# Kernel tuning notes

Hardware: AMD Instinct MI355X
Metric: run time of the kernel (lower is better)

The kernel has to match this reference:

```python
import jax, jax.numpy as jnp
import numpy as np

B, T, C, H = 4, 2048, 768, 12
HD = C // H  # 64
EPS = 1e-5


def layer_norm(x, g, b):
    mu = jnp.mean(x, axis=-1, keepdims=True)
    var = jnp.var(x, axis=-1, keepdims=True)
    return (x - mu) * jax.lax.rsqrt(var + EPS) * g + b


def setup_inputs() -> dict:
    key = jax.random.key(0)
    ks = jax.random.split(key, 14)
    s_c = 1.0 / np.sqrt(C)
    s_4c = 1.0 / np.sqrt(4 * C)
    return {
        "x": jax.random.normal(ks[0], (B, T, C), jnp.float32),
        # per-head Q/K/V projections stacked over heads [H, C, HD]
        "wq": jax.random.uniform(ks[1], (H, C, HD), jnp.float32, -s_c, s_c),
        "bq": jnp.zeros((H, HD), jnp.float32),
        "wk": jax.random.uniform(ks[2], (H, C, HD), jnp.float32, -s_c, s_c),
        "bk": jnp.zeros((H, HD), jnp.float32),
        "wv": jax.random.uniform(ks[3], (H, C, HD), jnp.float32, -s_c, s_c),
        "bv": jnp.zeros((H, HD), jnp.float32),
        "w_proj": jax.random.uniform(ks[4], (C, C), jnp.float32, -s_c, s_c),
        "b_proj": jnp.zeros((C,), jnp.float32),
        "w1": jax.random.uniform(ks[5], (C, 4 * C), jnp.float32, -s_c, s_c),
        "b1": jnp.zeros((4 * C,), jnp.float32),
        "w2": jax.random.uniform(ks[6], (4 * C, C), jnp.float32, -s_4c, s_4c),
        "b2": jnp.zeros((C,), jnp.float32),
        "g1": jnp.ones((C,), jnp.float32),
        "beta1": jnp.zeros((C,), jnp.float32),
        "g2": jnp.ones((C,), jnp.float32),
        "beta2": jnp.zeros((C,), jnp.float32),
    }


def reference(x, wq, bq, wk, bk, wv, bv, w_proj, b_proj, w1, b1, w2, b2, g1, beta1, g2, beta2):
    # --- attention sublayer ---
    h = layer_norm(x, g1, beta1)
    q = jnp.einsum('btc,hcd->bhtd', h, wq) + bq[None, :, None, :]
    k = jnp.einsum('btc,hcd->bhtd', h, wk) + bk[None, :, None, :]
    v = jnp.einsum('btc,hcd->bhtd', h, wv) + bv[None, :, None, :]
    # NOTE: source applies NO 1/sqrt(head_size) scaling
    scores = jnp.einsum('bhtd,bhsd->bhts', q, k)  # [B,H,T,T]
    causal = jnp.tril(jnp.ones((T, T), bool))
    scores = jnp.where(causal, scores, -jnp.inf)
    wei = jax.nn.softmax(scores, axis=-1)
    attn = jnp.einsum('bhts,bhsd->bhtd', wei, v)  # [B,H,T,HD]
    attn = attn.transpose(0, 2, 1, 3).reshape(B, T, C)  # concat heads
    x = x + attn @ w_proj + b_proj
    # --- MLP sublayer ---
    h2 = layer_norm(x, g2, beta2)
    x = x + jax.nn.relu(h2 @ w1 + b1) @ w2 + b2
    return x
```

## Files before the change

kernel.cpp:

```cpp
#include <hip/hip_runtime.h>
#include <hip/hip_bf16.h>
#include <math.h>

#define BB 4
#define TT 2048
#define CC 768
#define HH 12
#define HDIM 64
#define C4 3072
#define MM (BB*TT)
#define EPSL 1e-5f

typedef __bf16 bf16x8 __attribute__((ext_vector_type(8)));
typedef __bf16 bf16x4 __attribute__((ext_vector_type(4)));
typedef float f32x4 __attribute__((ext_vector_type(4)));

__device__ __forceinline__ ushort f2bf(float f) {
    union { float f; unsigned u; } v; v.f = f;
    unsigned r = v.u + 0x7fffu + ((v.u >> 16) & 1u);
    return (ushort)(r >> 16);
}

__device__ __forceinline__ void glds16(const void* g, void* l) {
    __builtin_amdgcn_global_load_lds(
        (const __attribute__((address_space(1))) void*)g,
        (__attribute__((address_space(3))) void*)l, 16, 0, 0);
}

#define WVM(N) asm volatile("s_waitcnt vmcnt(" #N ")" ::: "memory")
#define WLG0   asm volatile("s_waitcnt lgkmcnt(0)" ::: "memory")

__device__ __forceinline__ void pbar() {
    __builtin_amdgcn_sched_barrier(0);
    __builtin_amdgcn_s_barrier();
    __builtin_amdgcn_sched_barrier(0);
}

__global__ __launch_bounds__(256) void ln_k(const float* __restrict__ X,
                                            const float* __restrict__ G,
                                            const float* __restrict__ Be,
                                            ushort* __restrict__ O)
{
    int row = blockIdx.x;
    const float* xr = X + (size_t)row * CC;
    int t = threadIdx.x;
    float v0 = xr[t], v1 = xr[t + 256], v2 = xr[t + 512];
    float s  = v0 + v1 + v2;
    float sq = v0*v0 + v1*v1 + v2*v2;
    #pragma unroll
    for (int off = 32; off; off >>= 1) {
        s  += __shfl_xor(s,  off);
        sq += __shfl_xor(sq, off);
    }
    __shared__ float red[8];
    int wv = t >> 6, ln = t & 63;
    if (ln == 0) { red[wv] = s; red[4 + wv] = sq; }
    __syncthreads();
    s  = red[0] + red[1] + red[2] + red[3];
    sq = red[4] + red[5] + red[6] + red[7];
    float mu  = s * (1.0f / CC);
    float var = sq * (1.0f / CC) - mu * mu;
    float rs  = rsqrtf(var + EPSL);
    ushort* orow = O + (size_t)row * CC;
    orow[t]       = f2bf((v0 - mu) * rs * G[t]       + Be[t]);
    orow[t + 256] = f2bf((v1 - mu) * rs * G[t + 256] + Be[t + 256]);
    orow[t + 512] = f2bf((v2 - mu) * rs * G[t + 512] + Be[t + 512]);
}

__global__ __launch_bounds__(256) void ln_add_k(float* __restrict__ X,
                                                const float* __restrict__ P,
                                                const float* __restrict__ G,
                                                const float* __restrict__ Be,
                                                ushort* __restrict__ O)
{
    int row = blockIdx.x;
    float* xr = X + (size_t)row * CC;
    const float* pr = P + (size_t)row * CC;
    int t = threadIdx.x;
    float v0 = xr[t]       + pr[t];
    float v1 = xr[t + 256] + pr[t + 256];
    float v2 = xr[t + 512] + pr[t + 512];
    xr[t] = v0; xr[t + 256] = v1; xr[t + 512] = v2;
    float s  = v0 + v1 + v2;
    float sq = v0*v0 + v1*v1 + v2*v2;
    #pragma unroll
    for (int off = 32; off; off >>= 1) {
        s  += __shfl_xor(s,  off);
        sq += __shfl_xor(sq, off);
    }
    __shared__ float red[8];
    int wv = t >> 6, ln = t & 63;
    if (ln == 0) { red[wv] = s; red[4 + wv] = sq; }
    __syncthreads();
    s  = red[0] + red[1] + red[2] + red[3];
    sq = red[4] + red[5] + red[6] + red[7];
    float mu  = s * (1.0f / CC);
    float var = sq * (1.0f / CC) - mu * mu;
    float rs  = rsqrtf(var + EPSL);
    ushort* orow = O + (size_t)row * CC;
    orow[t]       = f2bf((v0 - mu) * rs * G[t]       + Be[t]);
    orow[t + 256] = f2bf((v1 - mu) * rs * G[t + 256] + Be[t + 256]);
    orow[t + 512] = f2bf((v2 - mu) * rs * G[t + 512] + Be[t + 512]);
}

__global__ __launch_bounds__(256) void addto_k(float* __restrict__ o,
                                               const float* __restrict__ p,
                                               int n4)
{
    int i = blockIdx.x * 256 + threadIdx.x;
    int stride = gridDim.x * 256;
    for (; i < n4; i += stride) {
        float4 a = ((const float4*)o)[i];
        float4 b = ((const float4*)p)[i];
        a.x += b.x; a.y += b.y; a.z += b.z; a.w += b.w;
        ((float4*)o)[i] = a;
    }
}

template<int MODE>
__global__ __launch_bounds__(256) void repack_k(const float* __restrict__ W,
                                                ushort* __restrict__ WT,
                                                int K, int N, int outStride)
{
    __shared__ float tl[64][65];
    int n0 = blockIdx.x * 64, k0 = blockIdx.y * 64;
    int c = threadIdx.x & 63, rr = threadIdx.x >> 6;
    #pragma unroll
    for (int i = 0; i < 16; ++i) {
        int r = i * 4 + rr;
        float v;
        if (MODE == 0) v = W[(size_t)(k0 + r) * N + n0 + c];
        else           v = W[((size_t)(n0 >> 6) * CC + k0 + r) * 64 + c];
        tl[r][c] = v;
    }
    __syncthreads();
    #pragma unroll
    for (int i = 0; i < 16; ++i) {
        int r = i * 4 + rr;
        WT[(size_t)(n0 + r) * outStride + k0 + c] = f2bf(tl[c][r]);
    }
}

template<int EPI>
__global__ __launch_bounds__(512, 2) void gemm8p(
    const ushort* __restrict__ A, const ushort* __restrict__ BT,
    int M, int N, int K,
    void* __restrict__ ov0, void* __restrict__ ov1, void* __restrict__ ov2,
    const float* __restrict__ bias0, const float* __restrict__ bias1,
    const float* __restrict__ bias2,
    const float* __restrict__ resid, ushort* __restrict__ obf,
    float* __restrict__ part)
{
    __shared__ ushort lds[2][2][256 * 64];

    int nbx = gridDim.x;
    int nwg = nbx * gridDim.y * gridDim.z;
    int orig = (blockIdx.z * gridDim.y + blockIdx.y) * nbx + blockIdx.x;
    int cpx = nwg >> 3;
    int swz = (orig & 7) * cpx + (orig >> 3);
    int zi = swz / (nbx * gridDim.y);
    int rem = swz - zi * nbx * gridDim.y;
    int bn = rem % nbx, bm = rem / nbx;

    int tid = threadIdx.x;
    int lane = tid & 63;
    int w = tid >> 6;
    int wrow = (w >> 2) * 128, wcol = (w & 3) * 64;
    int fr = lane & 15, kh = lane >> 4;
    int rxor = (fr & 7) * 8;

    const size_t aR0 = (size_t)bm * 256;
    const size_t bR0 = (size_t)bn * 256;
    const int Ksl = K / (int)gridDim.z;
    const int koff = zi * Ksl;
    const int nt = Ksl >> 6;

    int srow = tid >> 3;
    int scol = (tid & 7) * 8;
    int gcol = koff + (scol ^ ((srow & 7) * 8));

    f32x4 acc[8][4] = {};

    {
        glds16(BT + (bR0 +   0 + srow) * K + gcol, &lds[0][1][(  0 + srow) * 64 + scol]);
        glds16(BT + (bR0 +  64 + srow) * K + gcol, &lds[0][1][( 64 + srow) * 64 + scol]);
        glds16(BT + (bR0 + 128 + srow) * K + gcol, &lds[0][1][(128 + srow) * 64 + scol]);
        glds16(BT + (bR0 + 192 + srow) * K + gcol, &lds[0][1][(192 + srow) * 64 + scol]);
        glds16(A  + (aR0 +   0 + srow) * K + gcol, &lds[0][0][(  0 + srow) * 64 + scol]);
        glds16(A  + (aR0 + 128 + srow) * K + gcol, &lds[0][0][(128 + srow) * 64 + scol]);
        glds16(A  + (aR0 +  64 + srow) * K + gcol, &lds[0][0][( 64 + srow) * 64 + scol]);
        glds16(A  + (aR0 + 192 + srow) * K + gcol, &lds[0][0][(192 + srow) * 64 + scol]);
    }
    WVM(2);
    pbar();

    for (int t = 0; t < nt; ++t) {
        int slot = t & 1, nslot = slot ^ 1;
        int kst = gcol + ((t + 1) << 6);
        bool st = (t + 1) < nt;
        const ushort* Asl = &lds[slot][0][0];
        const ushort* Bsl = &lds[slot][1][0];
        bf16x8 aF[4][2];
        #pragma unroll
        for (int p = 0; p < 4; ++p) {
            const int rh = p >> 1, ch = p & 1;
            if (ch == 0) {
                #pragma unroll
                for (int i = 0; i < 4; ++i)
                    #pragma unroll
                    for (int k2 = 0; k2 < 2; ++k2) {
                        int R = wrow + rh * 64 + i * 16 + fr;
                        aF[i][k2] = *(const bf16x8*)&Asl[R * 64 + ((k2 * 32 + kh * 8) ^ rxor)];
                    }
            }
            bf16x8 bF[2][2];
            #pragma unroll
            for (int j2 = 0; j2 < 2; ++j2)
                #pragma unroll
                for (int k2 = 0; k2 < 2; ++k2) {
                    int Rb = wcol + ch * 32 + j2 * 16 + fr;
                    bF[j2][k2] = *(const bf16x8*)&Bsl[Rb * 64 + ((k2 * 32 + kh * 8) ^ rxor)];
                }
            if (st) {
                if (p == 0) {
                    glds16(BT + (bR0 +   0 + srow) * K + kst, &lds[nslot][1][(  0 + srow) * 64 + scol]);
                    glds16(BT + (bR0 +  64 + srow) * K + kst, &lds[nslot][1][( 64 + srow) * 64 + scol]);
                    glds16(BT + (bR0 + 128 + srow) * K + kst, &lds[nslot][1][(128 + srow) * 64 + scol]);
                    glds16(BT + (bR0 + 192 + srow) * K + kst, &lds[nslot][1][(192 + srow) * 64 + scol]);
                } else if (p == 1) {
                    glds16(A  + (aR0 +   0 + srow) * K + kst, &lds[nslot][0][(  0 + srow) * 64 + scol]);
                    glds16(A  + (aR0 + 128 + srow) * K + kst, &lds[nslot][0][(128 + srow) * 64 + scol]);
                    glds16(A  + (aR0 +  64 + srow) * K + kst, &lds[nslot][0][( 64 + srow) * 64 + scol]);
                    glds16(A  + (aR0 + 192 + srow) * K + kst, &lds[nslot][0][(192 + srow) * 64 + scol]);
                }
            }
            __builtin_amdgcn_s_setprio(1);
            #pragma unroll
            for (int i = 0; i < 4; ++i)
                #pragma unroll
                for (int j2 = 0; j2 < 2; ++j2)
                    #pragma unroll
                    for (int k2 = 0; k2 < 2; ++k2)
                        acc[rh * 4 + i][ch * 2 + j2] = __builtin_amdgcn_mfma_f32_16x16x32_bf16(
                            aF[i][k2], bF[j2][k2], acc[rh * 4 + i][ch * 2 + j2], 0, 0, 0);
            __builtin_amdgcn_s_setprio(0);
            if (p == 1) { if (st) { WVM(8); } else { WVM(0); } }
            else if (p == 3) { if (st) { WVM(2); } }
            WLG0;
            pbar();
        }
    }

    if (gridDim.z > 1 && zi > 0) {
        #pragma unroll
        for (int ri = 0; ri < 8; ++ri) {
            int row0 = bm * 256 + wrow + ri * 16 + kh * 4;
            #pragma unroll
            for (int cj = 0; cj < 4; ++cj) {
                int col = bn * 256 + wcol + cj * 16 + fr;
                #pragma unroll
                for (int r = 0; r < 4; ++r)
                    part[(size_t)(row0 + r) * N + col] = acc[ri][cj][r];
            }
        }
    } else if (EPI == 1) {
        int seg = bn / 3;
        ushort* op = (ushort*)(seg == 0 ? ov0 : (seg == 1 ? ov1 : ov2));
        const float* bsp = seg == 0 ? bias0 : (seg == 1 ? bias1 : bias2);
        int cb = (bn - seg * 3) * 256 + wcol;
        int h = cb >> 6;
        #pragma unroll
        for (int ri = 0; ri < 8; ++ri) {
            int row0 = bm * 256 + wrow + ri * 16 + kh * 4;
            int b = row0 >> 11;
            int t0 = row0 & (TT - 1);
            #pragma unroll
            for (int cj = 0; cj < 4; ++cj) {
                int d = cj * 16 + fr;
                float bsv = bsp[h * 64 + d];
                #pragma unroll
                for (int r = 0; r < 4; ++r)
                    op[((size_t)(b * HH + h) * TT + t0 + r) * 64 + d] =
                        f2bf(acc[ri][cj][r] + bsv);
            }
        }
    } else if (EPI == 2) {
        float* o0 = (float*)ov0;
        #pragma unroll
        for (int ri = 0; ri < 8; ++ri) {
            int row0 = bm * 256 + wrow + ri * 16 + kh * 4;
            #pragma unroll
            for (int cj = 0; cj < 4; ++cj) {
                int col = bn * 256 + wcol + cj * 16 + fr;
                float bsv = bias0[col];
                #pragma unroll
                for (int r = 0; r < 4; ++r) {
                    size_t idx = (size_t)(row0 + r) * N + col;
                    o0[idx] = acc[ri][cj][r] + bsv + resid[idx];
                }
            }
        }
    } else {
        #pragma unroll
        for (int ri = 0; ri < 8; ++ri) {
            int row0 = bm * 256 + wrow + ri * 16 + kh * 4;
            #pragma unroll
            for (int cj = 0; cj < 4; ++cj) {
                int col = bn * 256 + wcol + cj * 16 + fr;
                float bsv = bias0[col];
                #pragma unroll
                for (int r = 0; r < 4; ++r) {
                    float v = fmaxf(acc[ri][cj][r] + bsv, 0.f);
                    obf[(size_t)(row0 + r) * N + col] = f2bf(v);
                }
            }
        }
    }
}

__global__ __launch_bounds__(256) void vtrans_k(const ushort* __restrict__ V,
                                                ushort* __restrict__ Vt)
{
    __shared__ ushort tl[64][72];
    int blk = blockIdx.x;
    int tt = blk & 31, bh = blk >> 5;
    size_t base = (size_t)bh * TT * 64;
    int t0 = tt * 64;
    int e = threadIdx.x;
    int rr = e >> 3, cc8 = (e & 7) * 8;
    #pragma unroll
    for (int p = 0; p < 2; ++p) {
        int t = p * 32 + rr;
        *(uint4*)&tl[t][cc8] = *(const uint4*)&V[base + (size_t)(t0 + t) * 64 + cc8];
    }
    __syncthreads();
    #pragma unroll
    for (int p = 0; p < 2; ++p) {
        int d = p * 32 + rr;
        ushort tmp[8];
        #pragma unroll
        for (int i = 0; i < 8; ++i) tmp[i] = tl[cc8 + i][d];
        *(uint4*)&Vt[base + (size_t)d * TT + t0 + cc8] = *(uint4*)tmp;
    }
}

__global__ __launch_bounds__(256) void attn_k(const ushort* __restrict__ Q,
                                              const ushort* __restrict__ Kb,
                                              const ushort* __restrict__ Vt,
                                              ushort* __restrict__ Ob)
{
    __shared__ ushort Kl[64][72];
    __shared__ ushort Vl[64][72];
    __shared__ ushort Pl[4][16][68];

    int orig = blockIdx.x;
    int swz = (orig & 7) * 192 + (orig >> 3);
    int qt = 31 - (swz & 31);
    int bh = swz >> 5;
    int b = bh / HH, h = bh - b * HH;
    int q0 = qt * 64;
    int tid = threadIdx.x, lane = tid & 63, w = tid >> 6;
    int c = lane & 15, g = lane >> 4;
    size_t base = (size_t)bh * TT * 64;
    int srow = tid >> 3, scol = (tid & 7) * 8;
    const float LOG2E = 1.44269504088896340736f;

    bf16x8 aq[2];
    #pragma unroll
    for (int kc = 0; kc < 2; ++kc) {
        bf16x8 raw = *(const bf16x8*)&Q[base + (size_t)(q0 + w * 16 + c) * 64 + kc * 32 + g * 8];
        #pragma unroll
        for (int e = 0; e < 8; ++e)
            raw[e] = (__bf16)((float)raw[e] * LOG2E);
        aq[kc] = raw;
    }

    f32x4 oa[4] = {};
    float mrun[4] = {-INFINITY, -INFINITY, -INFINITY, -INFINITY};
    float lrun[4] = {0.f, 0.f, 0.f, 0.f};

    for (int kv0 = 0; kv0 <= q0; kv0 += 64) {
        __syncthreads();
        #pragma unroll
        for (int p = 0; p < 2; ++p) {
            int r = p * 32 + srow;
            *(uint4*)&Kl[r][scol] = *(const uint4*)&Kb[base + (size_t)(kv0 + r) * 64 + scol];
            *(uint4*)&Vl[r][scol] = *(const uint4*)&Vt[base + (size_t)r * TT + kv0 + scol];
        }
        __syncthreads();

        f32x4 sa[4] = {};
        #pragma unroll
        for (int kc = 0; kc < 2; ++kc)
            #pragma unroll
            for (int j = 0; j < 4; ++j) {
                bf16x8 kf = *(const bf16x8*)&Kl[j * 16 + c][kc * 32 + g * 8];
                sa[j] = __builtin_amdgcn_mfma_f32_16x16x32_bf16(aq[kc], kf, sa[j], 0, 0, 0);
            }

        if (kv0 == q0) {
            #pragma unroll
            for (int j = 0; j < 4; ++j)
                #pragma unroll
                for (int r = 0; r < 4; ++r)
                    if (j * 16 + c > w * 16 + g * 4 + r) sa[j][r] = -1e30f;
        }

        float vlmax = sa[0][0];
        #pragma unroll
        for (int j = 0; j < 4; ++j)
            #pragma unroll
            for (int r = 0; r < 4; ++r) vlmax = fmaxf(vlmax, sa[j][r]);
        float mmin = fminf(fminf(mrun[0], mrun[1]), fminf(mrun[2], mrun[3]));
        if (!__all(vlmax <= mmin + 11.5f)) {
            #pragma unroll
            for (int r = 0; r < 4; ++r) {
                float m0 = fmaxf(fmaxf(sa[0][r], sa[1][r]), fmaxf(sa[2][r], sa[3][r]));
                #pragma unroll
                for (int off = 8; off; off >>= 1) m0 = fmaxf(m0, __shfl_xor(m0, off));
                float mnew = fmaxf(mrun[r], m0);
                float sc = __builtin_amdgcn_exp2f(mrun[r] - mnew);
                lrun[r] *= sc;
                #pragma unroll
                for (int j = 0; j < 4; ++j) oa[j][r] *= sc;
                mrun[r] = mnew;
            }
        }
        #pragma unroll
        for (int r = 0; r < 4; ++r) {
            float ps = 0.f;
            #pragma unroll
            for (int j = 0; j < 4; ++j) {
                float p = __builtin_amdgcn_exp2f(sa[j][r] - mrun[r]);
                sa[j][r] = p;
                ps += p;
            }
            lrun[r] += ps;
        }

        #pragma unroll
        for (int r = 0; r < 4; ++r)
            #pragma unroll
            for (int j = 0; j < 4; ++j)
                Pl[w][g * 4 + r][j * 16 + c] = (ushort)__builtin_bit_cast(unsigned short, (__bf16)sa[j][r]);

        bf16x8 pf[2];
        #pragma unroll
        for (int kc = 0; kc < 2; ++kc) {
            bf16x4 lo = *(const bf16x4*)&Pl[w][c][kc * 32 + g * 8];
            bf16x4 hi = *(const bf16x4*)&Pl[w][c][kc * 32 + g * 8 + 4];
            pf[kc] = __builtin_shufflevector(lo, hi, 0, 1, 2, 3, 4, 5, 6, 7);
        }

        #pragma unroll
        for (int kc = 0; kc < 2; ++kc)
            #pragma unroll
            for (int j = 0; j < 4; ++j) {
                bf16x8 vf = *(const bf16x8*)&Vl[j * 16 + c][kc * 32 + g * 8];
                oa[j] = __builtin_amdgcn_mfma_f32_16x16x32_bf16(pf[kc], vf, oa[j], 0, 0, 0);
            }
    }

    float inv[4];
    #pragma unroll
    for (int r = 0; r < 4; ++r) {
        float l = lrun[r];
        #pragma unroll
        for (int off = 8; off; off >>= 1) l += __shfl_xor(l, off);
        inv[r] = 1.0f / l;
    }
    size_t orow = (size_t)b * TT + q0 + w * 16;
    #pragma unroll
    for (int j = 0; j < 4; ++j)
        #pragma unroll
        for (int r = 0; r < 4; ++r) {
            float v = oa[j][r] * inv[r];
            Ob[(orow + g * 4 + r) * CC + h * 64 + j * 16 + c] = f2bf(v);
        }
}

extern "C" void kernel_launch(void* const* d_in, const int* in_sizes, int n_in,
                              void* d_out, int out_size, void* d_ws, size_t ws_size,
                              hipStream_t stream)
{
    const float* x   = (const float*)d_in[0];
    const float* wq  = (const float*)d_in[1];
    const float* bq  = (const float*)d_in[2];
    const float* wk  = (const float*)d_in[3];
    const float* bk  = (const float*)d_in[4];
    const float* wvw = (const float*)d_in[5];
    const float* bv  = (const float*)d_in[6];
    const float* wp  = (const float*)d_in[7];
    const float* bp  = (const float*)d_in[8];
    const float* w1  = (const float*)d_in[9];
    const float* b1  = (const float*)d_in[10];
    const float* w2  = (const float*)d_in[11];
    const float* b2  = (const float*)d_in[12];
    const float* g1  = (const float*)d_in[13];
    const float* be1 = (const float*)d_in[14];
    const float* g2  = (const float*)d_in[15];
    const float* be2 = (const float*)d_in[16];

    float* out = (float*)d_out;
    const size_t S = (size_t)MM * CC;

    ushort* wsu   = (ushort*)d_ws;
    ushort* WTqkv = wsu;
    ushort* WTp   = WTqkv + (size_t)2304 * 768;
    ushort* WT1   = WTp   + (size_t)768 * 768;
    ushort* WT2   = WT1   + (size_t)3072 * 768;
    ushort* hbf   = WT2   + (size_t)768 * 3072;
    ushort* attnb = hbf   + S;
    ushort* qb    = attnb + S;
    ushort* kb    = qb + S;
    ushort* vb    = kb + S;
    ushort* vtb   = vb + S;
    ushort* midb  = qb;
    float*  part_proj = (float*)qb;
    float*  part_w2   = (float*)hbf;

    dim3 rg(12, 12);
    repack_k<1><<<rg, 256, 0, stream>>>(wq,  WTqkv,                      768, 768, 768);
    repack_k<1><<<rg, 256, 0, stream>>>(wk,  WTqkv + (size_t)768*768,    768, 768, 768);
    repack_k<1><<<rg, 256, 0, stream>>>(wvw, WTqkv + (size_t)2*768*768,  768, 768, 768);
    repack_k<0><<<rg, 256, 0, stream>>>(wp,  WTp, 768, 768, 768);
    repack_k<0><<<dim3(48, 12), 256, 0, stream>>>(w1, WT1, 768, 3072, 768);
    repack_k<0><<<dim3(12, 48), 256, 0, stream>>>(w2, WT2, 3072, 768, 3072);

    ln_k<<<MM, 256, 0, stream>>>(x, g1, be1, hbf);
    gemm8p<1><<<dim3(9, 32, 1), 512, 0, stream>>>(hbf, WTqkv, MM, 2304, CC,
        qb, kb, vb, bq, bk, bv, nullptr, nullptr, nullptr);
    vtrans_k<<<48 * 32, 256, 0, stream>>>(vb, vtb);
    attn_k<<<48 * 32, 256, 0, stream>>>(qb, kb, vtb, attnb);
    gemm8p<2><<<dim3(3, 32, 2), 512, 0, stream>>>(attnb, WTp, MM, CC, CC,
        out, nullptr, nullptr, bp, nullptr, nullptr, x, nullptr, part_proj);

    ln_add_k<<<MM, 256, 0, stream>>>(out, part_proj, g2, be2, hbf);
    gemm8p<3><<<dim3(12, 32, 1), 512, 0, stream>>>(hbf, WT1, MM, C4, CC,
        nullptr, nullptr, nullptr, b1, nullptr, nullptr, nullptr, midb, nullptr);
    gemm8p<2><<<dim3(3, 32, 2), 512, 0, stream>>>(midb, WT2, MM, CC, C4,
        out, nullptr, nullptr, b2, nullptr, nullptr, out, nullptr, part_w2);
    addto_k<<<2048, 256, 0, stream>>>(out, part_w2, MM * CC / 4);
}
```

Baseline: 311.0 us.

## Pair causal query tiles per block, prefetch K/V into registers, swizzle LDS

```diff
diff --git a/kernel.cpp b/kernel.cpp
--- a/kernel.cpp
+++ b/kernel.cpp
@@ -349,134 +349,153 @@
                                               const ushort* __restrict__ Vt,
                                               ushort* __restrict__ Ob)
 {
-    __shared__ ushort Kl[64][72];
-    __shared__ ushort Vl[64][72];
+    __shared__ ushort Kl[64][64];
+    __shared__ ushort Vl[64][64];
     __shared__ ushort Pl[4][16][68];
 
     int orig = blockIdx.x;
-    int swz = (orig & 7) * 192 + (orig >> 3);
-    int qt = 31 - (swz & 31);
-    int bh = swz >> 5;
+    int swz = (orig & 7) * 96 + (orig >> 3);
+    int pair = swz & 15;
+    int bh = swz >> 4;
     int b = bh / HH, h = bh - b * HH;
-    int q0 = qt * 64;
     int tid = threadIdx.x, lane = tid & 63, w = tid >> 6;
     int c = lane & 15, g = lane >> 4;
     size_t base = (size_t)bh * TT * 64;
-    int srow = tid >> 3, scol = (tid & 7) * 8;
+    int srow = tid >> 3;
+    int scol = (tid & 7) * 8;
+    int sw0 = scol ^ ((srow & 7) * 8);
+    int sw1 = scol ^ (((srow + 32) & 7) * 8);
+    int rxk = (c & 7) * 8;
     const float LOG2E = 1.44269504088896340736f;
 
-    bf16x8 aq[2];
-    #pragma unroll
-    for (int kc = 0; kc < 2; ++kc) {
-        bf16x8 raw = *(const bf16x8*)&Q[base + (size_t)(q0 + w * 16 + c) * 64 + kc * 32 + g * 8];
-        #pragma unroll
-        for (int e = 0; e < 8; ++e)
-            raw[e] = (__bf16)((float)raw[e] * LOG2E);
-        aq[kc] = raw;
-    }
-
-    f32x4 oa[4] = {};
-    float mrun[4] = {-INFINITY, -INFINITY, -INFINITY, -INFINITY};
-    float lrun[4] = {0.f, 0.f, 0.f, 0.f};
-
-    for (int kv0 = 0; kv0 <= q0; kv0 += 64) {
-        __syncthreads();
-        #pragma unroll
-        for (int p = 0; p < 2; ++p) {
-            int r = p * 32 + srow;
-            *(uint4*)&Kl[r][scol] = *(const uint4*)&Kb[base + (size_t)(kv0 + r) * 64 + scol];
-            *(uint4*)&Vl[r][scol] = *(const uint4*)&Vt[base + (size_t)r * TT + kv0 + scol];
-        }
-        __syncthreads();
-
-        f32x4 sa[4] = {};
-        #pragma unroll
-        for (int kc = 0; kc < 2; ++kc)
-            #pragma unroll
-            for (int j = 0; j < 4; ++j) {
-                bf16x8 kf = *(const bf16x8*)&Kl[j * 16 + c][kc * 32 + g * 8];
-                sa[j] = __builtin_amdgcn_mfma_f32_16x16x32_bf16(aq[kc], kf, sa[j], 0, 0, 0);
-            }
-
-        if (kv0 == q0) {
+    #pragma unroll
+    for (int sel = 0; sel < 2; ++sel) {
+        int qt = sel ? (31 - pair) : pair;
+        int q0 = qt * 64;
+
+        bf16x8 aq[2];
+        #pragma unroll
+        for (int kc = 0; kc < 2; ++kc) {
+            bf16x8 raw = *(const bf16x8*)&Q[base + (size_t)(q0 + w * 16 + c) * 64 + kc * 32 + g * 8];
+            #pragma unroll
+            for (int e = 0; e < 8; ++e)
+                raw[e] = (__bf16)((float)raw[e] * LOG2E);
+            aq[kc] = raw;
+        }
+
+        f32x4 oa[4] = {};
+        float mrun[4] = {-INFINITY, -INFINITY, -INFINITY, -INFINITY};
+        float lrun[4] = {0.f, 0.f, 0.f, 0.f};
+
+        uint4 k0r = *(const uint4*)&Kb[base + (size_t)srow * 64 + scol];
+        uint4 k1r = *(const uint4*)&Kb[base + (size_t)(32 + srow) * 64 + scol];
+        uint4 v0r = *(const uint4*)&Vt[base + (size_t)srow * TT + scol];
+        uint4 v1r = *(const uint4*)&Vt[base + (size_t)(32 + srow) * TT + scol];
+
+        for (int kv0 = 0; kv0 <= q0; kv0 += 64) {
+            __syncthreads();
+            *(uint4*)&Kl[srow][sw0]      = k0r;
+            *(uint4*)&Kl[32 + srow][sw1] = k1r;
+            *(uint4*)&Vl[srow][sw0]      = v0r;
+            *(uint4*)&Vl[32 + srow][sw1] = v1r;
+            __syncthreads();
+            if (kv0 + 64 <= q0) {
+                int kn = kv0 + 64;
+                k0r = *(const uint4*)&Kb[base + (size_t)(kn + srow) * 64 + scol];
+                k1r = *(const uint4*)&Kb[base + (size_t)(kn + 32 + srow) * 64 + scol];
+                v0r = *(const uint4*)&Vt[base + (size_t)srow * TT + kn + scol];
+                v1r = *(const uint4*)&Vt[base + (size_t)(32 + srow) * TT + kn + scol];
+            }
+
+            f32x4 sa[4] = {};
+            #pragma unroll
+            for (int kc = 0; kc < 2; ++kc)
+                #pragma unroll
+                for (int j = 0; j < 4; ++j) {
+                    bf16x8 kf = *(const bf16x8*)&Kl[j * 16 + c][(kc * 32 + g * 8) ^ rxk];
+                    sa[j] = __builtin_amdgcn_mfma_f32_16x16x32_bf16(aq[kc], kf, sa[j], 0, 0, 0);
+                }
+
+            if (kv0 == q0) {
+                #pragma unroll
+                for (int j = 0; j < 4; ++j)
+                    #pragma unroll
+                    for (int r = 0; r < 4; ++r)
+                        if (j * 16 + c > w * 16 + g * 4 + r) sa[j][r] = -1e30f;
+            }
+
+            float vlmax = sa[0][0];
             #pragma unroll
             for (int j = 0; j < 4; ++j)
                 #pragma unroll
-                for (int r = 0; r < 4; ++r)
-                    if (j * 16 + c > w * 16 + g * 4 + r) sa[j][r] = -1e30f;
-        }
-
-        float vlmax = sa[0][0];
+                for (int r = 0; r < 4; ++r) vlmax = fmaxf(vlmax, sa[j][r]);
+            float mmin = fminf(fminf(mrun[0], mrun[1]), fminf(mrun[2], mrun[3]));
+            if (!__all(vlmax <= mmin + 11.5f)) {
+                #pragma unroll
+                for (int r = 0; r < 4; ++r) {
+                    float m0 = fmaxf(fmaxf(sa[0][r], sa[1][r]), fmaxf(sa[2][r], sa[3][r]));
+                    #pragma unroll
+                    for (int off = 8; off; off >>= 1) m0 = fmaxf(m0, __shfl_xor(m0, off));
+                    float mnew = fmaxf(mrun[r], m0);
+                    float sc = __builtin_amdgcn_exp2f(mrun[r] - mnew);
+                    lrun[r] *= sc;
+                    #pragma unroll
+                    for (int j = 0; j < 4; ++j) oa[j][r] *= sc;
+                    mrun[r] = mnew;
+                }
+            }
+            #pragma unroll
+            for (int r = 0; r < 4; ++r) {
+                float ps = 0.f;
+                #pragma unroll
+                for (int j = 0; j < 4; ++j) {
+                    float p = __builtin_amdgcn_exp2f(sa[j][r] - mrun[r]);
+                    sa[j][r] = p;
+                    ps += p;
+                }
+                lrun[r] += ps;
+            }
+
+            #pragma unroll
+            for (int r = 0; r < 4; ++r)
+                #pragma unroll
+                for (int j = 0; j < 4; ++j)
+                    Pl[w][g * 4 + r][j * 16 + c] = (ushort)__builtin_bit_cast(unsigned short, (__bf16)sa[j][r]);
+
+            bf16x8 pf[2];
+            #pragma unroll
+            for (int kc = 0; kc < 2; ++kc) {
+                bf16x4 lo = *(const bf16x4*)&Pl[w][c][kc * 32 + g * 8];
+                bf16x4 hi = *(const bf16x4*)&Pl[w][c][kc * 32 + g * 8 + 4];
+                pf[kc] = __builtin_shufflevector(lo, hi, 0, 1, 2, 3, 4, 5, 6, 7);
+            }
+
+            #pragma unroll
+            for (int kc = 0; kc < 2; ++kc)
+                #pragma unroll
+                for (int j = 0; j < 4; ++j) {
+                    bf16x8 vf = *(const bf16x8*)&Vl[j * 16 + c][(kc * 32 + g * 8) ^ rxk];
+                    oa[j] = __builtin_amdgcn_mfma_f32_16x16x32_bf16(pf[kc], vf, oa[j], 0, 0, 0);
+                }
+        }
+
+        float inv[4];
+        #pragma unroll
+        for (int r = 0; r < 4; ++r) {
+            float l = lrun[r];
+            #pragma unroll
+            for (int off = 8; off; off >>= 1) l += __shfl_xor(l, off);
+            inv[r] = 1.0f / l;
+        }
+        size_t orow = (size_t)b * TT + q0 + w * 16;
         #pragma unroll
         for (int j = 0; j < 4; ++j)
             #pragma unroll
-            for (int r = 0; r < 4; ++r) vlmax = fmaxf(vlmax, sa[j][r]);
-        float mmin = fminf(fminf(mrun[0], mrun[1]), fminf(mrun[2], mrun[3]));
-        if (!__all(vlmax <= mmin + 11.5f)) {
-            #pragma unroll
             for (int r = 0; r < 4; ++r) {
-                float m0 = fmaxf(fmaxf(sa[0][r], sa[1][r]), fmaxf(sa[2][r], sa[3][r]));
-                #pragma unroll
-                for (int off = 8; off; off >>= 1) m0 = fmaxf(m0, __shfl_xor(m0, off));
-                float mnew = fmaxf(mrun[r], m0);
-                float sc = __builtin_amdgcn_exp2f(mrun[r] - mnew);
-                lrun[r] *= sc;
-                #pragma unroll
-                for (int j = 0; j < 4; ++j) oa[j][r] *= sc;
-                mrun[r] = mnew;
-            }
-        }
-        #pragma unroll
-        for (int r = 0; r < 4; ++r) {
-            float ps = 0.f;
-            #pragma unroll
-            for (int j = 0; j < 4; ++j) {
-                float p = __builtin_amdgcn_exp2f(sa[j][r] - mrun[r]);
-                sa[j][r] = p;
-                ps += p;
-            }
-            lrun[r] += ps;
-        }
-
-        #pragma unroll
-        for (int r = 0; r < 4; ++r)
-            #pragma unroll
-            for (int j = 0; j < 4; ++j)
-                Pl[w][g * 4 + r][j * 16 + c] = (ushort)__builtin_bit_cast(unsigned short, (__bf16)sa[j][r]);
-
-        bf16x8 pf[2];
-        #pragma unroll
-        for (int kc = 0; kc < 2; ++kc) {
-            bf16x4 lo = *(const bf16x4*)&Pl[w][c][kc * 32 + g * 8];
-            bf16x4 hi = *(const bf16x4*)&Pl[w][c][kc * 32 + g * 8 + 4];
-            pf[kc] = __builtin_shufflevector(lo, hi, 0, 1, 2, 3, 4, 5, 6, 7);
-        }
-
-        #pragma unroll
-        for (int kc = 0; kc < 2; ++kc)
-            #pragma unroll
-            for (int j = 0; j < 4; ++j) {
-                bf16x8 vf = *(const bf16x8*)&Vl[j * 16 + c][kc * 32 + g * 8];
-                oa[j] = __builtin_amdgcn_mfma_f32_16x16x32_bf16(pf[kc], vf, oa[j], 0, 0, 0);
-            }
-    }
-
-    float inv[4];
-    #pragma unroll
-    for (int r = 0; r < 4; ++r) {
-        float l = lrun[r];
-        #pragma unroll
-        for (int off = 8; off; off >>= 1) l += __shfl_xor(l, off);
-        inv[r] = 1.0f / l;
-    }
-    size_t orow = (size_t)b * TT + q0 + w * 16;
-    #pragma unroll
-    for (int j = 0; j < 4; ++j)
-        #pragma unroll
-        for (int r = 0; r < 4; ++r) {
-            float v = oa[j][r] * inv[r];
-            Ob[(orow + g * 4 + r) * CC + h * 64 + j * 16 + c] = f2bf(v);
-        }
+                float v = oa[j][r] * inv[r];
+                Ob[(orow + g * 4 + r) * CC + h * 64 + j * 16 + c] = f2bf(v);
+            }
+    }
 }
 
 extern "C" void kernel_launch(void* const* d_in, const int* in_sizes, int n_in,
@@ -531,7 +550,7 @@
     gemm8p<1><<<dim3(9, 32, 1), 512, 0, stream>>>(hbf, WTqkv, MM, 2304, CC,
         qb, kb, vb, bq, bk, bv, nullptr, nullptr, nullptr);
     vtrans_k<<<48 * 32, 256, 0, stream>>>(vb, vtb);
-    attn_k<<<48 * 32, 256, 0, stream>>>(qb, kb, vtb, attnb);
+    attn_k<<<48 * 16, 256, 0, stream>>>(qb, kb, vtb, attnb);
     gemm8p<2><<<dim3(3, 32, 2), 512, 0, stream>>>(attnb, WTp, MM, CC, CC,
         out, nullptr, nullptr, bp, nullptr, nullptr, x, nullptr, part_proj);
 
```

Measured after the change: 299.7 us. -3.7%, faster.
